# Optimization experiments

Measured on AMD Instinct MI355X. Metric: run time of the kernel, lower is better.

Reference implementation:

```python
import jax, jax.numpy as jnp
import numpy as np

K = 10

def _lrelu(v):
    return jax.nn.leaky_relu(v, negative_slope=0.2)

def _knn_idx(x, k):
    # x: [B, C, N]; returns indices of k nearest neighbors [B, N, k]
    xx = jnp.sum(x * x, axis=1, keepdims=True)          # [B,1,N]
    inner = -2.0 * jnp.einsum('bcn,bcm->bnm', x, x)     # [B,N,N]
    pd = -xx - inner - jnp.swapaxes(xx, 1, 2)           # -squared distance [B,N,N]
    _, idx = jax.lax.top_k(pd, k)
    return idx

def _graph_feature(x, k):
    # x: [B, C, N] -> edge features [B, 2C, N, k]
    idx = _knn_idx(x, k)                                # [B,N,k]
    xt = jnp.swapaxes(x, 1, 2)                          # [B,N,C]
    feat = jax.vmap(lambda xb, ib: xb[ib])(xt, idx)     # [B,N,k,C] gather
    center = xt[:, :, None, :]                          # [B,N,1,C]
    f = jnp.concatenate([feat - center,
                         jnp.broadcast_to(center, feat.shape)], axis=-1)  # [B,N,k,2C]
    return jnp.transpose(f, (0, 3, 1, 2))               # [B,2C,N,k]

def _edge_block(x, W, k):
    # conv2d 1x1 (no bias) + LeakyReLU + max over neighbors
    g = _graph_feature(x, k)                            # [B,2C,N,k]
    h = _lrelu(jnp.einsum('oc,bcnk->bonk', W, g))
    return jnp.max(h, axis=-1)                          # [B,O,N]

def setup_inputs() -> dict:
    key = jax.random.key(0)
    ks = jax.random.split(key, 9)
    def w(k_, *shape):
        fan_in = shape[-1]
        return jax.random.normal(k_, shape, dtype=jnp.float32) / np.sqrt(fan_in)
    return {
        'x':  jax.random.normal(ks[0], (8, 3, 2048), dtype=jnp.float32),
        'W1': w(ks[1], 64, 6),
        'W2': w(ks[2], 64, 128),
        'W3': w(ks[3], 128, 128),
        'W4': w(ks[4], 256, 256),
        'W5': w(ks[5], 512, 512),
        'L1': w(ks[6], 512, 1024),
        'L2': w(ks[7], 256, 512),
        'b2': jnp.zeros((256,), dtype=jnp.float32),
    }

def reference(x, W1, W2, W3, W4, W5, L1, L2, b2):
    x1 = _edge_block(x,  W1, K)   # [B,64,N]
    x2 = _edge_block(x1, W2, K)   # [B,64,N]
    x3 = _edge_block(x2, W3, K)   # [B,128,N]
    x4 = _edge_block(x3, W4, K)   # [B,256,N]
    h = jnp.concatenate([x1, x2, x3, x4], axis=1)        # [B,512,N]
    h = _lrelu(jnp.einsum('oc,bcn->bon', W5, h))         # [B,512,N]
    hmax = jnp.max(h, axis=-1)                           # [B,512]
    havg = jnp.mean(h, axis=-1)                          # [B,512]
    f = jnp.concatenate([hmax, havg], axis=1)            # [B,1024]
    f = _lrelu(f @ L1.T)                                 # [B,512]
    out = _lrelu(f @ L2.T + b2)                          # [B,256]
    return out
```

## Files before the change

kernel.cpp:

```cpp
#include <hip/hip_runtime.h>
#include <cstdint>
#include <cstddef>

constexpr int B_ = 8;
constexpr int N_ = 2048;
constexpr int K_ = 10;

typedef __attribute__((ext_vector_type(8))) short bf16x8;
typedef __attribute__((ext_vector_type(4))) float f32x4;

__device__ __forceinline__ float lrelu(float v) { return fmaxf(v, 0.2f * v); }

__device__ __forceinline__ short f2bf(float f) {
    uint32_t u = __builtin_bit_cast(uint32_t, f);
    u += 0x7fff + ((u >> 16) & 1);
    return (short)(u >> 16);
}
__device__ __forceinline__ float bf2f(short s) {
    uint32_t x = ((uint32_t)(unsigned short)s) << 16;
    return __builtin_bit_cast(float, x);
}

__global__ void k_transpose(const float* __restrict__ x, float* __restrict__ xt) {
    int i = blockIdx.x * 256 + threadIdx.x;
    if (i >= B_ * N_) return;
    int b = i / N_, n = i % N_;
#pragma unroll
    for (int c = 0; c < 3; ++c)
        xt[(size_t)i * 3 + c] = x[((size_t)b * 3 + c) * N_ + n];
}

__global__ void k_cvt(const float* __restrict__ W4, const float* __restrict__ W5,
                      short* __restrict__ Wb4, short* __restrict__ W5b) {
    int i = blockIdx.x * 256 + threadIdx.x;
    if (i < 256 * 128) {
        Wb4[i] = f2bf(W4[(size_t)(i >> 7) * 256 + (i & 127)]);
    } else {
        int k = i - 256 * 128;
        if (k < 512 * 512) W5b[k] = f2bf(W5[k]);
    }
}

__global__ void k_cvt2(const float* __restrict__ W2, const float* __restrict__ W3,
                       short* __restrict__ w2h, short* __restrict__ w2l,
                       short* __restrict__ w3h, short* __restrict__ w3l) {
    int i = blockIdx.x * 256 + threadIdx.x;
    if (i < 64 * 64) {
        float v = W2[(size_t)(i >> 6) * 128 + (i & 63)];
        short h = f2bf(v);
        w2h[i] = h; w2l[i] = f2bf(v - bf2f(h));
    } else if (i < 64 * 64 + 128 * 64) {
        int k = i - 64 * 64;
        float v = W3[(size_t)(k >> 6) * 128 + (k & 63)];
        short h = f2bf(v);
        w3h[k] = h; w3l[k] = f2bf(v - bf2f(h));
    }
}

__global__ void k_norms(const float* __restrict__ xt, int LD, int OFF, int C,
                        float* __restrict__ nrm) {
    int gid = blockIdx.x * 256 + threadIdx.x;
    int wid = gid >> 6;
    int lane = threadIdx.x & 63;
    if (wid >= B_ * N_) return;
    const float* row = xt + (size_t)wid * LD + OFF;
    float s = 0.f;
    for (int c = lane; c < C; c += 64) { float v = row[c]; s += v * v; }
#pragma unroll
    for (int off = 32; off; off >>= 1) s += __shfl_down(s, off);
    if (lane == 0) nrm[wid] = s;
}

__global__ __launch_bounds__(256) void k_knn3(const float* __restrict__ x,
                                              int* __restrict__ idxout) {
    __shared__ float xs[3][N_];
    __shared__ float ns[N_];
    const int b = blockIdx.x;
    const int w = threadIdx.x >> 6, lane = threadIdx.x & 63;
    const int n = blockIdx.y * 4 + w;
    for (int e = threadIdx.x; e < 3 * N_; e += 256)
        xs[e / N_][e % N_] = x[(size_t)b * 3 * N_ + e];
    __syncthreads();
    for (int m = threadIdx.x; m < N_; m += 256) {
        float a0 = xs[0][m], a1 = xs[1][m], a2 = xs[2][m];
        ns[m] = a0 * a0 + a1 * a1 + a2 * a2;
    }
    __syncthreads();
    const float q0 = xs[0][n], q1 = xs[1][n], q2 = xs[2][n];

    float sv[32];
#pragma unroll
    for (int g = 0; g < 32; ++g) {
        int m = g * 64 + lane;
        sv[g] = 2.f * (q0 * xs[0][m] + q1 * xs[1][m] + q2 * xs[2][m]) - ns[m];
    }
    float lm = sv[0];
#pragma unroll
    for (int g = 1; g < 32; ++g) lm = fmaxf(lm, sv[g]);
    float cur = lm, T = lm;
#pragma unroll
    for (int i = 0; i < K_; ++i) {
        float wm = cur;
#pragma unroll
        for (int off = 1; off < 64; off <<= 1) wm = fmaxf(wm, __shfl_xor(wm, off));
        T = wm;
        unsigned long long m = __ballot(cur == wm);
        int first = __ffsll(m) - 1;
        if (lane == first) cur = -INFINITY;
    }
    float kv[K_]; int ki[K_];
#pragma unroll
    for (int i = 0; i < K_; ++i) { kv[i] = -INFINITY; ki[i] = 0x7fffffff; }
#pragma unroll
    for (int g = 0; g < 32; ++g) {
        unsigned long long mk = __ballot(sv[g] >= T && sv[g] > kv[0]);
        while (mk) {
            int l = __ffsll(mk) - 1;
            mk &= mk - 1;
            float v = __shfl(sv[g], l);
            if (v > kv[0]) {
                kv[0] = v; ki[0] = g * 64 + l;
#pragma unroll
                for (int u = 0; u < K_ - 1; ++u)
                    if (kv[u] > kv[u + 1]) {
                        float tv = kv[u]; kv[u] = kv[u + 1]; kv[u + 1] = tv;
                        int tix = ki[u]; ki[u] = ki[u + 1]; ki[u + 1] = tix;
                    }
            }
        }
    }
    if (lane == 0) {
        int* op = idxout + ((size_t)b * N_ + n) * K_;
#pragma unroll
        for (int k = 0; k < K_; ++k) op[k] = ki[K_ - 1 - k];
    }
}

template <int C>
__global__ __launch_bounds__(256) void k_scores_mfma(const float* __restrict__ xt, int LD, int OFF,
                                                     const float* __restrict__ nrm,
                                                     float* __restrict__ S, int b0) {
    constexpr int RPC = C / 64;
    constexpr int NCH = 3 * RPC;
    constexpr int T = N_ / 64;
    __shared__ short AN[64 * 64];
    __shared__ short AM[64 * 64];
    const int bl = blockIdx.x;
    const int b = b0 + bl;
    int p = blockIdx.y;
    int r0 = 0, off = 0;
    while (off + (T - r0) <= p) { off += T - r0; ++r0; }
    const int ti = r0, tj = r0 + (p - off);
    const int n0 = ti * 64, m0 = tj * 64;
    const int t = threadIdx.x;
    const int lane = t & 63, w = t >> 6;
    const int colg = lane & 15, kg = lane >> 4;
    const float* xb = xt + ((size_t)b * N_) * LD + OFF;
    const float* nb = nrm + (size_t)b * N_;
    float* Sb = S + (size_t)bl * N_ * N_;

    f32x4 acc[4];
#pragma unroll
    for (int j = 0; j < 4; ++j) acc[j] = (f32x4){0.f, 0.f, 0.f, 0.f};

    for (int ch = 0; ch < NCH; ++ch) {
        const int region = ch / RPC;
        const int cc0 = (ch % RPC) * 64;
        __syncthreads();
#pragma unroll
        for (int e = 0; e < 4; ++e) {
            int idx = t + e * 256;
            int r = idx >> 4, q = idx & 15;
            float4 vn = *(const float4*)&xb[(size_t)(n0 + r) * LD + cc0 + q * 4];
            float4 vm = *(const float4*)&xb[(size_t)(m0 + r) * LD + cc0 + q * 4];
            float an4[4] = {vn.x, vn.y, vn.z, vn.w};
            float am4[4] = {vm.x, vm.y, vm.z, vm.w};
            short sa[4], sb[4];
#pragma unroll
            for (int c2 = 0; c2 < 4; ++c2) {
                short hn = f2bf(an4[c2]);
                short hm = f2bf(am4[c2]);
                sa[c2] = (region == 1) ? f2bf(an4[c2] - bf2f(hn)) : hn;
                sb[c2] = (region == 2) ? f2bf(am4[c2] - bf2f(hm)) : hm;
            }
            int base16 = r * 128 + (q >> 1) * 16;
            int byte = (base16 ^ ((r & 7) << 4)) + (q & 1) * 8;
            *(short4*)((char*)AN + byte) = make_short4(sa[0], sa[1], sa[2], sa[3]);
            *(short4*)((char*)AM + byte) = make_short4(sb[0], sb[1], sb[2], sb[3]);
        }
        __syncthreads();
        const int arow = w * 16 + colg;
#pragma unroll
        for (int s = 0; s < 2; ++s) {
            int abyte = (arow * 128 + s * 64 + kg * 16) ^ ((arow & 7) << 4);
            bf16x8 af = *(const bf16x8*)((const char*)AN + abyte);
#pragma unroll
            for (int j = 0; j < 4; ++j) {
                int brow = j * 16 + colg;
                int bbyte = (brow * 128 + s * 64 + kg * 16) ^ ((brow & 7) << 4);
                bf16x8 bfr = *(const bf16x8*)((const char*)AM + bbyte);
                acc[j] = __builtin_amdgcn_mfma_f32_16x16x32_bf16(af, bfr, acc[j], 0, 0, 0);
            }
        }
    }
#pragma unroll
    for (int j = 0; j < 4; ++j) {
        float nm = nb[m0 + j * 16 + colg];
#pragma unroll
        for (int r = 0; r < 4; ++r) {
            int row = n0 + w * 16 + kg * 4 + r;
            Sb[(size_t)row * N_ + m0 + j * 16 + colg] = 2.f * acc[j][r] - nm;
        }
    }
    if (ti != tj) {
#pragma unroll
        for (int r = 0; r < 4; ++r) {
            int nrow = n0 + w * 16 + kg * 4 + r;
            float nn = nb[nrow];
#pragma unroll
            for (int j = 0; j < 4; ++j)
                Sb[(size_t)(m0 + j * 16 + colg) * N_ + nrow] = 2.f * acc[j][r] - nn;
        }
    }
}

__global__ __launch_bounds__(256) void k_topk(const float* __restrict__ S,
                                              int* __restrict__ idxout, int b0) {
    const int bl = blockIdx.x, b = b0 + bl;
    const int wv = threadIdx.x >> 6, lane = threadIdx.x & 63;
    const int n = blockIdx.y * 4 + wv;
    const float* row = S + (size_t)bl * N_ * N_ + (size_t)n * N_;

    float sv[32];
#pragma unroll
    for (int g = 0; g < 32; ++g) sv[g] = __builtin_nontemporal_load(&row[g * 64 + lane]);

    float lm = sv[0];
#pragma unroll
    for (int g = 1; g < 32; ++g) lm = fmaxf(lm, sv[g]);

    float cur = lm, T = lm;
#pragma unroll
    for (int i = 0; i < K_; ++i) {
        float wm = cur;
#pragma unroll
        for (int off = 1; off < 64; off <<= 1) wm = fmaxf(wm, __shfl_xor(wm, off));
        T = wm;
        unsigned long long m = __ballot(cur == wm);
        int first = __ffsll(m) - 1;
        if (lane == first) cur = -INFINITY;
    }

    float kv[K_]; int ki[K_];
#pragma unroll
    for (int i = 0; i < K_; ++i) { kv[i] = -INFINITY; ki[i] = 0x7fffffff; }

#pragma unroll
    for (int g = 0; g < 32; ++g) {
        unsigned long long mk = __ballot(sv[g] >= T && sv[g] > kv[0]);
        while (mk) {
            int l = __ffsll(mk) - 1;
            mk &= mk - 1;
            float v = __shfl(sv[g], l);
            if (v > kv[0]) {
                kv[0] = v; ki[0] = g * 64 + l;
#pragma unroll
                for (int u = 0; u < K_ - 1; ++u)
                    if (kv[u] > kv[u + 1]) {
                        float tv = kv[u]; kv[u] = kv[u + 1]; kv[u + 1] = tv;
                        int tix = ki[u]; ki[u] = ki[u + 1]; ki[u + 1] = tix;
                    }
            }
        }
    }
    if (lane == 0) {
        int* op = idxout + ((size_t)b * N_ + n) * K_;
#pragma unroll
        for (int k = 0; k < K_; ++k) op[k] = ki[K_ - 1 - k];
    }
}

template <int C, int O>
__global__ __launch_bounds__(256) void k_center(const float* __restrict__ xt, int LD, int OFF,
                                                const float* __restrict__ W,
                                                float* __restrict__ tbuf) {
    constexpr int KC = (C == 3) ? 4 : 32;
    __shared__ __align__(16) float XT[64][36];
    __shared__ __align__(16) float WDT[KC][68];
    const int b = blockIdx.x;
    const int n0 = blockIdx.y * 64;
    const int ob = blockIdx.z * 64;
    const int t = threadIdx.x;
    const int tn = t & 15, to = t >> 4;
    const float* xb = xt + ((size_t)b * N_) * LD + OFF;
    float4 acc[4];
#pragma unroll
    for (int i = 0; i < 4; ++i) acc[i] = make_float4(0, 0, 0, 0);
    for (int c0 = 0; c0 < C; c0 += KC) {
        __syncthreads();
        for (int e = t; e < 64 * KC; e += 256) {
            int r = e / KC, cc = e % KC;
            XT[r][cc] = (C == 3) ? ((cc < 3) ? xb[(size_t)(n0 + r) * LD + cc] : 0.f)
                                 : xb[(size_t)(n0 + r) * LD + c0 + cc];
        }
        for (int e = t; e < 64 * KC; e += 256) {
            int oo = e / KC, cc = e % KC;
            float wd, wc;
            if (C == 3) {
                wd = (cc < 3) ? W[(ob + oo) * 6 + cc] : 0.f;
                wc = (cc < 3) ? W[(ob + oo) * 6 + 3 + cc] : 0.f;
            } else {
                wd = W[(size_t)(ob + oo) * (2 * C) + c0 + cc];
                wc = W[(size_t)(ob + oo) * (2 * C) + C + c0 + cc];
            }
            WDT[cc][oo] = wc - wd;
        }
        __syncthreads();
#pragma unroll 4
        for (int cc = 0; cc < KC; ++cc) {
            float4 w4 = *(const float4*)&WDT[cc][to * 4];
#pragma unroll
            for (int i = 0; i < 4; ++i) {
                float a = XT[tn * 4 + i][cc];
                acc[i].x += a * w4.x; acc[i].y += a * w4.y;
                acc[i].z += a * w4.z; acc[i].w += a * w4.w;
            }
        }
    }
#pragma unroll
    for (int i = 0; i < 4; ++i)
        *(float4*)&tbuf[((size_t)b * N_ + n0 + tn * 4 + i) * O + ob + to * 4] = acc[i];
}

template <int C, int O>
__global__ __launch_bounds__(256) void k_conv(const float* __restrict__ xt, int LDI, int OFFI,
                                              const int* __restrict__ idx,
                                              const float* __restrict__ W,
                                              const float* __restrict__ tbuf,
                                              float* __restrict__ hout, int OFFO) {
    constexpr int KC = (C == 3) ? 4 : 32;
    __shared__ __align__(16) float A[160][36];
    __shared__ __align__(16) float WT[KC][68];
    __shared__ int nb_s[160];
    const int b = blockIdx.x;
    const int n0 = blockIdx.y * 16;
    const int t = threadIdx.x;
    const int p = t >> 4, og = t & 15;
    if (t < 160) nb_s[t] = idx[((size_t)b * N_ + n0 + t / K_) * K_ + (t % K_)];
    const float* xb = xt + ((size_t)b * N_) * LDI + OFFI;

    for (int ob = 0; ob < O; ob += 64) {
        float4 acc[K_];
#pragma unroll
        for (int j = 0; j < K_; ++j) acc[j] = make_float4(0, 0, 0, 0);
        for (int c0 = 0; c0 < C; c0 += KC) {
            __syncthreads();
            if (C == 3) {
                for (int e = t; e < 160 * 4; e += 256) {
                    int r = e / 4, cc = e % 4;
                    A[r][cc] = (cc < 3) ? xb[(size_t)nb_s[r] * LDI + cc] : 0.f;
                }
            } else {
                for (int e = t; e < 160 * 8; e += 256) {
                    int r = e / 8, c4 = e % 8;
                    *(float4*)&A[r][c4 * 4] =
                        *(const float4*)&xb[(size_t)nb_s[r] * LDI + c0 + c4 * 4];
                }
            }
            for (int e = t; e < 64 * KC; e += 256) {
                int oo = e / KC, cc = e % KC;
                float w;
                if (C == 3) w = (cc < 3) ? W[(ob + oo) * 6 + cc] : 0.f;
                else        w = W[(size_t)(ob + oo) * (2 * C) + c0 + cc];
                WT[cc][oo] = w;
            }
            __syncthreads();
#pragma unroll 4
            for (int cc = 0; cc < KC; ++cc) {
                float4 w4 = *(const float4*)&WT[cc][og * 4];
#pragma unroll
                for (int j = 0; j < K_; ++j) {
                    float a = A[p * K_ + j][cc];
                    acc[j].x += a * w4.x; acc[j].y += a * w4.y;
                    acc[j].z += a * w4.z; acc[j].w += a * w4.w;
                }
            }
        }
        float4 tv = *(const float4*)&tbuf[((size_t)b * N_ + n0 + p) * O + ob + og * 4];
        float4 mx = acc[0];
#pragma unroll
        for (int j = 1; j < K_; ++j) {
            mx.x = fmaxf(mx.x, acc[j].x); mx.y = fmaxf(mx.y, acc[j].y);
            mx.z = fmaxf(mx.z, acc[j].z); mx.w = fmaxf(mx.w, acc[j].w);
        }
        float4 r;
        r.x = lrelu(mx.x + tv.x); r.y = lrelu(mx.y + tv.y);
        r.z = lrelu(mx.z + tv.z); r.w = lrelu(mx.w + tv.w);
        *(float4*)&hout[((size_t)b * N_ + n0 + p) * 512 + OFFO + ob + og * 4] = r;
    }
}

template <int O>
__global__ __launch_bounds__(256) void k_conv23_mfma(const float* __restrict__ hcat, int OFFI,
                                                     const int* __restrict__ idx,
                                                     const short* __restrict__ Wh,
                                                     const short* __restrict__ Wl,
                                                     const float* __restrict__ tbuf,
                                                     float* __restrict__ hout, int OFFO) {
    constexpr int CT = O / 64;
    __shared__ short Ah[160 * 64];
    __shared__ short Al[160 * 64];
    __shared__ int nb_s[160];
    const int b = blockIdx.x;
    const int n0 = blockIdx.y * 16;
    const int t = threadIdx.x;
    const int lane = t & 63, wv = t >> 6;
    const int colg = lane & 15, kg = lane >> 4;
    if (t < 160) nb_s[t] = idx[((size_t)b * N_ + n0 + t / K_) * K_ + (t % K_)];
    __syncthreads();
    for (int e = t; e < 160 * 16; e += 256) {
        int r = e >> 4, q = e & 15;
        const float4 v = *(const float4*)&hcat[((size_t)b * N_ + nb_s[r]) * 512 + OFFI + q * 4];
        float a4[4] = {v.x, v.y, v.z, v.w};
        short sh[4], sl[4];
#pragma unroll
        for (int c2 = 0; c2 < 4; ++c2) {
            sh[c2] = f2bf(a4[c2]);
            sl[c2] = f2bf(a4[c2] - bf2f(sh[c2]));
        }
        int byte = r * 128 + ((q * 8) ^ (((r / K_) & 7) << 4));
        *(short4*)((char*)Ah + byte) = make_short4(sh[0], sh[1], sh[2], sh[3]);
        *(short4*)((char*)Al + byte) = make_short4(sl[0], sl[1], sl[2], sl[3]);
    }
    bf16x8 bh[CT][2], blo[CT][2];
    const int obase = wv * (O / 4);
#pragma unroll
    for (int ct = 0; ct < CT; ++ct)
#pragma unroll
        for (int ks = 0; ks < 2; ++ks) {
            int o = obase + ct * 16 + colg;
            bh[ct][ks]  = *(const bf16x8*)&Wh[(size_t)o * 64 + ks * 32 + kg * 8];
            blo[ct][ks] = *(const bf16x8*)&Wl[(size_t)o * 64 + ks * 32 + kg * 8];
        }
    __syncthreads();

    f32x4 macc[CT];
#pragma unroll
    for (int ct = 0; ct < CT; ++ct)
        macc[ct] = (f32x4){-INFINITY, -INFINITY, -INFINITY, -INFINITY};

    const int aswz = (colg & 7) << 4;
#pragma unroll
    for (int j = 0; j < K_; ++j) {
        const int arow = colg * K_ + j;
        bf16x8 afh[2], afl[2];
#pragma unroll
        for (int ks = 0; ks < 2; ++ks) {
            int byte = arow * 128 + ((ks * 64 + kg * 16) ^ aswz);
            afh[ks] = *(const bf16x8*)((const char*)Ah + byte);
            afl[ks] = *(const bf16x8*)((const char*)Al + byte);
        }
        f32x4 acc[CT];
#pragma unroll
        for (int ct = 0; ct < CT; ++ct) acc[ct] = (f32x4){0.f, 0.f, 0.f, 0.f};
#pragma unroll
        for (int ks = 0; ks < 2; ++ks)
#pragma unroll
            for (int ct = 0; ct < CT; ++ct)
                acc[ct] = __builtin_amdgcn_mfma_f32_16x16x32_bf16(afh[ks], bh[ct][ks], acc[ct], 0, 0, 0);
#pragma unroll
        for (int ks = 0; ks < 2; ++ks)
#pragma unroll
            for (int ct = 0; ct < CT; ++ct)
                acc[ct] = __builtin_amdgcn_mfma_f32_16x16x32_bf16(afl[ks], bh[ct][ks], acc[ct], 0, 0, 0);
#pragma unroll
        for (int ks = 0; ks < 2; ++ks)
#pragma unroll
            for (int ct = 0; ct < CT; ++ct)
                acc[ct] = __builtin_amdgcn_mfma_f32_16x16x32_bf16(afh[ks], blo[ct][ks], acc[ct], 0, 0, 0);
#pragma unroll
        for (int ct = 0; ct < CT; ++ct) {
            macc[ct].x = fmaxf(macc[ct].x, acc[ct].x);
            macc[ct].y = fmaxf(macc[ct].y, acc[ct].y);
            macc[ct].z = fmaxf(macc[ct].z, acc[ct].z);
            macc[ct].w = fmaxf(macc[ct].w, acc[ct].w);
        }
    }
#pragma unroll
    for (int ct = 0; ct < CT; ++ct)
#pragma unroll
        for (int r = 0; r < 4; ++r) {
            int p = kg * 4 + r;
            int o = obase + ct * 16 + colg;
            float v = macc[ct][r] + tbuf[((size_t)b * N_ + n0 + p) * O + o];
            hout[((size_t)b * N_ + n0 + p) * 512 + OFFO + o] = lrelu(v);
        }
}

__global__ __launch_bounds__(256) void k_conv4_mfma(const float* __restrict__ hcat,
                                                    const int* __restrict__ idx,
                                                    const short* __restrict__ Wb,
                                                    const float* __restrict__ tbuf,
                                                    float* __restrict__ hout) {
    __shared__ short Ab[160 * 128];
    __shared__ int nb_s[160];
    const int b = blockIdx.x;
    const int n0 = blockIdx.y * 16;
    const int t = threadIdx.x;
    const int lane = t & 63, wv = t >> 6;
    const int colg = lane & 15, kg = lane >> 4;
    if (t < 160) nb_s[t] = idx[((size_t)b * N_ + n0 + t / K_) * K_ + (t % K_)];
    __syncthreads();
    for (int e = t; e < 160 * 32; e += 256) {
        int r = e >> 5, q = e & 31;
        const float4 v = *(const float4*)&hcat[((size_t)b * N_ + nb_s[r]) * 512 + 128 + q * 4];
        short4 s4 = { f2bf(v.x), f2bf(v.y), f2bf(v.z), f2bf(v.w) };
        int byte = r * 256 + ((q * 8) ^ (((r / K_) & 7) << 4));
        *(short4*)((char*)Ab + byte) = s4;
    }
    bf16x8 bf[4][4];
    const int ob = wv * 64;
#pragma unroll
    for (int nt = 0; nt < 4; ++nt)
#pragma unroll
        for (int ks = 0; ks < 4; ++ks)
            bf[nt][ks] = *(const bf16x8*)&Wb[(size_t)(ob + nt * 16 + colg) * 128 + ks * 32 + kg * 8];
    __syncthreads();

    f32x4 macc[4];
#pragma unroll
    for (int nt = 0; nt < 4; ++nt)
        macc[nt] = (f32x4){-INFINITY, -INFINITY, -INFINITY, -INFINITY};

    const int arow = colg * K_;
    const int aswz = (colg & 7) << 4;
#pragma unroll
    for (int j = 0; j < K_; ++j) {
        f32x4 acc[4];
#pragma unroll
        for (int nt = 0; nt < 4; ++nt) acc[nt] = (f32x4){0.f, 0.f, 0.f, 0.f};
#pragma unroll
        for (int ks = 0; ks < 4; ++ks) {
            int byte = (arow + j) * 256 + (((ks * 32 + kg * 8) * 2) ^ aswz);
            bf16x8 af = *(const bf16x8*)((const char*)Ab + byte);
#pragma unroll
            for (int nt = 0; nt < 4; ++nt)
                acc[nt] = __builtin_amdgcn_mfma_f32_16x16x32_bf16(af, bf[nt][ks], acc[nt], 0, 0, 0);
        }
#pragma unroll
        for (int nt = 0; nt < 4; ++nt) {
            macc[nt].x = fmaxf(macc[nt].x, acc[nt].x);
            macc[nt].y = fmaxf(macc[nt].y, acc[nt].y);
            macc[nt].z = fmaxf(macc[nt].z, acc[nt].z);
            macc[nt].w = fmaxf(macc[nt].w, acc[nt].w);
        }
    }
#pragma unroll
    for (int nt = 0; nt < 4; ++nt)
#pragma unroll
        for (int r = 0; r < 4; ++r) {
            int p = kg * 4 + r;
            int o = ob + nt * 16 + colg;
            float v = macc[nt][r] + tbuf[((size_t)b * N_ + n0 + p) * 256 + o];
            hout[((size_t)b * N_ + n0 + p) * 512 + 256 + o] = lrelu(v);
        }
}

__global__ __launch_bounds__(256) void k_final_mfma(const float* __restrict__ hcat,
                                                    const short* __restrict__ W5b,
                                                    float* __restrict__ pmax,
                                                    float* __restrict__ psum) {
    __shared__ short Ab[64 * 128];
    const int b = blockIdx.x, nc = blockIdx.y, obk = blockIdx.z;
    const int n0 = nc * 64, ob = obk * 64;
    const int t = threadIdx.x, lane = t & 63, wv = t >> 6;
    const int colg = lane & 15, kg = lane >> 4;
    const int o = ob + wv * 16 + colg;

    f32x4 acc[4];
#pragma unroll
    for (int mt = 0; mt < 4; ++mt) acc[mt] = (f32x4){0.f, 0.f, 0.f, 0.f};

    for (int kc = 0; kc < 4; ++kc) {
        __syncthreads();
        for (int e = t; e < 64 * 32; e += 256) {
            int r = e >> 5, q = e & 31;
            const float4 v = *(const float4*)&hcat[((size_t)b * N_ + n0 + r) * 512 + kc * 128 + q * 4];
            short4 s4 = { f2bf(v.x), f2bf(v.y), f2bf(v.z), f2bf(v.w) };
            int byte = r * 256 + ((q * 8) ^ ((r & 7) << 4));
            *(short4*)((char*)Ab + byte) = s4;
        }
        __syncthreads();
#pragma unroll
        for (int ks = 0; ks < 4; ++ks) {
            bf16x8 bfrag = *(const bf16x8*)&W5b[(size_t)o * 512 + kc * 128 + ks * 32 + kg * 8];
#pragma unroll
            for (int mt = 0; mt < 4; ++mt) {
                int row = mt * 16 + colg;
                int byte = row * 256 + (((ks * 32 + kg * 8) * 2) ^ ((row & 7) << 4));
                bf16x8 af = *(const bf16x8*)((const char*)Ab + byte);
                acc[mt] = __builtin_amdgcn_mfma_f32_16x16x32_bf16(af, bfrag, acc[mt], 0, 0, 0);
            }
        }
    }
    float mx = -INFINITY, sm = 0.f;
#pragma unroll
    for (int mt = 0; mt < 4; ++mt)
#pragma unroll
        for (int r = 0; r < 4; ++r) {
            float v = lrelu(acc[mt][r]);
            mx = fmaxf(mx, v); sm += v;
        }
    mx = fmaxf(mx, __shfl_xor(mx, 16)); sm += __shfl_xor(sm, 16);
    mx = fmaxf(mx, __shfl_xor(mx, 32)); sm += __shfl_xor(sm, 32);
    if (lane < 16) {
        pmax[((size_t)b * 512 + ob + wv * 16 + lane) * 32 + nc] = mx;
        psum[((size_t)b * 512 + ob + wv * 16 + lane) * 32 + nc] = sm;
    }
}

__global__ __launch_bounds__(256) void k_pool(const float* __restrict__ pmax,
                                              const float* __restrict__ psum,
                                              float* __restrict__ f) {
    int i = blockIdx.x * 256 + threadIdx.x;
    if (i >= B_ * 512) return;
    int b = i >> 9, o = i & 511;
    const float* pm = pmax + (size_t)i * 32;
    const float* ps = psum + (size_t)i * 32;
    float mm = -INFINITY, ss = 0.f;
#pragma unroll
    for (int q = 0; q < 32; ++q) { mm = fmaxf(mm, pm[q]); ss += ps[q]; }
    f[(size_t)b * 1024 + o] = mm;
    f[(size_t)b * 1024 + 512 + o] = ss * (1.0f / 2048.0f);
}

__global__ __launch_bounds__(256) void k_fc1(const float* __restrict__ f,
                                             const float* __restrict__ L1,
                                             float* __restrict__ f1) {
    __shared__ float fs[8][1024];
    const int t = threadIdx.x, lane = t & 63, w = t >> 6;
    for (int e = t; e < 2048; e += 256)
        *(float4*)&fs[0][e * 4] = *(const float4*)&f[e * 4];
    __syncthreads();
    const int o = blockIdx.x * 4 + w;
    float acc[8];
#pragma unroll
    for (int b = 0; b < 8; ++b) acc[b] = 0.f;
    const float* Lrow = L1 + (size_t)o * 1024;
#pragma unroll
    for (int e = 0; e < 16; ++e) {
        float wv = Lrow[e * 64 + lane];
#pragma unroll
        for (int b = 0; b < 8; ++b) acc[b] += wv * fs[b][e * 64 + lane];
    }
#pragma unroll
    for (int off = 32; off; off >>= 1)
#pragma unroll
        for (int b = 0; b < 8; ++b) acc[b] += __shfl_xor(acc[b], off);
#pragma unroll
    for (int b = 0; b < 8; ++b)
        if (lane == b) f1[(size_t)b * 512 + o] = lrelu(acc[b]);
}

__global__ __launch_bounds__(256) void k_fc2(const float* __restrict__ f1,
                                             const float* __restrict__ L2,
                                             const float* __restrict__ b2,
                                             float* __restrict__ out) {
    __shared__ float fs[8][512];
    const int t = threadIdx.x, lane = t & 63, w = t >> 6;
    for (int e = t; e < 1024; e += 256)
        *(float4*)&fs[0][e * 4] = *(const float4*)&f1[e * 4];
    __syncthreads();
    const int o = blockIdx.x * 4 + w;
    float acc[8];
#pragma unroll
    for (int b = 0; b < 8; ++b) acc[b] = 0.f;
    const float* Lrow = L2 + (size_t)o * 512;
#pragma unroll
    for (int e = 0; e < 8; ++e) {
        float wv = Lrow[e * 64 + lane];
#pragma unroll
        for (int b = 0; b < 8; ++b) acc[b] += wv * fs[b][e * 64 + lane];
    }
#pragma unroll
    for (int off = 32; off; off >>= 1)
#pragma unroll
        for (int b = 0; b < 8; ++b) acc[b] += __shfl_xor(acc[b], off);
    float bb = b2[o];
#pragma unroll
    for (int b = 0; b < 8; ++b)
        if (lane == b) out[(size_t)b * 256 + o] = lrelu(acc[b] + bb);
}

extern "C" void kernel_launch(void* const* d_in, const int* in_sizes, int n_in,
                              void* d_out, int out_size, void* d_ws, size_t ws_size,
                              hipStream_t stream) {
    (void)in_sizes; (void)n_in; (void)out_size;
    const float* x  = (const float*)d_in[0];
    const float* W1 = (const float*)d_in[1];
    const float* W2 = (const float*)d_in[2];
    const float* W3 = (const float*)d_in[3];
    const float* W4 = (const float*)d_in[4];
    const float* W5 = (const float*)d_in[5];
    const float* L1 = (const float*)d_in[6];
    const float* L2 = (const float*)d_in[7];
    const float* b2 = (const float*)d_in[8];
    float* out = (float*)d_out;

    float* ws   = (float*)d_ws;
    float* xt   = ws;
    float* nrm  = xt + (size_t)B_ * N_ * 3;
    int*   idxb = (int*)(nrm + (size_t)B_ * N_);
    float* tb   = (float*)(idxb + (size_t)B_ * N_ * K_);
    float* hcat = tb + (size_t)B_ * N_ * 256;
    float* pmax = hcat + (size_t)B_ * N_ * 512;
    float* psum = pmax + (size_t)B_ * 512 * 32;
    short* wb4  = (short*)(psum + (size_t)B_ * 512 * 32);
    short* w5b  = wb4 + 256 * 128;
    short* w2h  = w5b + 512 * 512;
    short* w2l  = w2h + 64 * 64;
    short* w3h  = w2l + 64 * 64;
    short* w3l  = w3h + 128 * 64;
    float* fbuf = (float*)(w3l + 128 * 64);
    float* f1b  = fbuf + 8192;
    float* scor = f1b + 4096;

    const size_t base_f = 49152 + 16384 + 163840 + 4194304 + 8388608 +
                          131072 + 131072 + 16384 + 131072 + 12288 + 8192 + 4096;
    const size_t nsq = (size_t)N_ * N_;
    size_t avail = (ws_size / 4 > base_f) ? (ws_size / 4 - base_f) : 0;
    int CH = 1;
    if (avail >= 8 * nsq) CH = 8;
    else if (avail >= 4 * nsq) CH = 4;
    else if (avail >= 2 * nsq) CH = 2;

    constexpr int TP = (N_ / 64) * (N_ / 64 + 1) / 2;

    dim3 blk(256);
    k_transpose<<<dim3((B_ * N_ + 255) / 256), blk, 0, stream>>>(x, xt);
    k_cvt<<<dim3((256 * 128 + 512 * 512 + 255) / 256), blk, 0, stream>>>(W4, W5, wb4, w5b);
    k_cvt2<<<dim3((64 * 64 + 128 * 64 + 255) / 256), blk, 0, stream>>>(W2, W3, w2h, w2l, w3h, w3l);

    k_knn3<<<dim3(B_, N_ / 4), blk, 0, stream>>>(x, idxb);
    k_center<3, 64><<<dim3(B_, N_ / 64, 1), blk, 0, stream>>>(xt, 3, 0, W1, tb);
    k_conv<3, 64><<<dim3(B_, N_ / 16), blk, 0, stream>>>(xt, 3, 0, idxb, W1, tb, hcat, 0);

    k_norms<<<dim3(B_ * N_ / 4), blk, 0, stream>>>(hcat, 512, 0, 64, nrm);
    for (int b0 = 0; b0 < B_; b0 += CH) {
        k_scores_mfma<64><<<dim3(CH, TP), blk, 0, stream>>>(hcat, 512, 0, nrm, scor, b0);
        k_topk<<<dim3(CH, N_ / 4), blk, 0, stream>>>(scor, idxb, b0);
    }
    k_center<64, 64><<<dim3(B_, N_ / 64, 1), blk, 0, stream>>>(hcat, 512, 0, W2, tb);
    k_conv23_mfma<64><<<dim3(B_, N_ / 16), blk, 0, stream>>>(hcat, 0, idxb, w2h, w2l, tb, hcat, 64);

    k_norms<<<dim3(B_ * N_ / 4), blk, 0, stream>>>(hcat, 512, 64, 64, nrm);
    for (int b0 = 0; b0 < B_; b0 += CH) {
        k_scores_mfma<64><<<dim3(CH, TP), blk, 0, stream>>>(hcat, 512, 64, nrm, scor, b0);
        k_topk<<<dim3(CH, N_ / 4), blk, 0, stream>>>(scor, idxb, b0);
    }
    k_center<64, 128><<<dim3(B_, N_ / 64, 2), blk, 0, stream>>>(hcat, 512, 64, W3, tb);
    k_conv23_mfma<128><<<dim3(B_, N_ / 16), blk, 0, stream>>>(hcat, 64, idxb, w3h, w3l, tb, hcat, 128);

    k_norms<<<dim3(B_ * N_ / 4), blk, 0, stream>>>(hcat, 512, 128, 128, nrm);
    for (int b0 = 0; b0 < B_; b0 += CH) {
        k_scores_mfma<128><<<dim3(CH, TP), blk, 0, stream>>>(hcat, 512, 128, nrm, scor, b0);
        k_topk<<<dim3(CH, N_ / 4), blk, 0, stream>>>(scor, idxb, b0);
    }
    k_center<128, 256><<<dim3(B_, N_ / 64, 4), blk, 0, stream>>>(hcat, 512, 128, W4, tb);
    k_conv4_mfma<<<dim3(B_, N_ / 16), blk, 0, stream>>>(hcat, idxb, wb4, tb, hcat);

    k_final_mfma<<<dim3(B_, 32, 8), blk, 0, stream>>>(hcat, w5b, pmax, psum);
    k_pool<<<dim3(B_ * 512 / 256), blk, 0, stream>>>(pmax, psum, fbuf);
    k_fc1<<<dim3(128), blk, 0, stream>>>(fbuf, L1, f1b);
    k_fc2<<<dim3(64), blk, 0, stream>>>(f1b, L2, b2, out);
}
```

Before: 524.0 us.

## Store kNN score matrix in bf16 and rerank candidates with exact fp32 distances

The pairwise score matrix written by the MFMA score kernel is now stored as bf16 instead of fp32, halving the N×N write and read traffic. The top-k kernel finds the 10th-largest bf16 score as a threshold. It then recomputes exact fp32 dot products against hcat for every candidate at or above that threshold, and selects the final neighbours from those exact values. The halved buffer also lets more batches fit per chunk. The risk is extra gather and shuffle-reduce work when many candidates tie near the threshold, plus possible misses if bf16 rounding pushes a true neighbour below the threshold.

```diff
diff --git a/kernel.cpp b/kernel.cpp
--- a/kernel.cpp
+++ b/kernel.cpp
@@ -18,6 +18,10 @@
 }
 __device__ __forceinline__ float bf2f(short s) {
     uint32_t x = ((uint32_t)(unsigned short)s) << 16;
+    return __builtin_bit_cast(float, x);
+}
+__device__ __forceinline__ float bf2fu(unsigned short u) {
+    uint32_t x = ((uint32_t)u) << 16;
     return __builtin_bit_cast(float, x);
 }
 
@@ -139,7 +143,7 @@
 template <int C>
 __global__ __launch_bounds__(256) void k_scores_mfma(const float* __restrict__ xt, int LD, int OFF,
                                                      const float* __restrict__ nrm,
-                                                     float* __restrict__ S, int b0) {
+                                                     unsigned short* __restrict__ S, int b0) {
     constexpr int RPC = C / 64;
     constexpr int NCH = 3 * RPC;
     constexpr int T = N_ / 64;
@@ -157,7 +161,7 @@
     const int colg = lane & 15, kg = lane >> 4;
     const float* xb = xt + ((size_t)b * N_) * LD + OFF;
     const float* nb = nrm + (size_t)b * N_;
-    float* Sb = S + (size_t)bl * N_ * N_;
+    unsigned short* Sb = S + (size_t)bl * N_ * N_;
 
     f32x4 acc[4];
 #pragma unroll
@@ -209,7 +213,7 @@
 #pragma unroll
         for (int r = 0; r < 4; ++r) {
             int row = n0 + w * 16 + kg * 4 + r;
-            Sb[(size_t)row * N_ + m0 + j * 16 + colg] = 2.f * acc[j][r] - nm;
+            Sb[(size_t)row * N_ + m0 + j * 16 + colg] = (unsigned short)f2bf(2.f * acc[j][r] - nm);
         }
     }
     if (ti != tj) {
@@ -219,26 +223,35 @@
             float nn = nb[nrow];
 #pragma unroll
             for (int j = 0; j < 4; ++j)
-                Sb[(size_t)(m0 + j * 16 + colg) * N_ + nrow] = 2.f * acc[j][r] - nn;
-        }
-    }
-}
-
-__global__ __launch_bounds__(256) void k_topk(const float* __restrict__ S,
+                Sb[(size_t)(m0 + j * 16 + colg) * N_ + nrow] = (unsigned short)f2bf(2.f * acc[j][r] - nn);
+        }
+    }
+}
+
+template <int C>
+__global__ __launch_bounds__(256) void k_topk(const unsigned short* __restrict__ S,
+                                              const float* __restrict__ hcat, int LD, int OFF,
+                                              const float* __restrict__ nrm,
                                               int* __restrict__ idxout, int b0) {
     const int bl = blockIdx.x, b = b0 + bl;
     const int wv = threadIdx.x >> 6, lane = threadIdx.x & 63;
     const int n = blockIdx.y * 4 + wv;
-    const float* row = S + (size_t)bl * N_ * N_ + (size_t)n * N_;
-
-    float sv[32];
-#pragma unroll
-    for (int g = 0; g < 32; ++g) sv[g] = __builtin_nontemporal_load(&row[g * 64 + lane]);
-
-    float lm = sv[0];
-#pragma unroll
-    for (int g = 1; g < 32; ++g) lm = fmaxf(lm, sv[g]);
-
+    const unsigned short* row = S + (size_t)bl * N_ * N_ + (size_t)n * N_;
+
+    float sv[8][4];
+#pragma unroll
+    for (int g = 0; g < 8; ++g) {
+        uint2 u = *(const uint2*)&row[g * 256 + lane * 4];
+        sv[g][0] = bf2fu((unsigned short)(u.x & 0xffffu));
+        sv[g][1] = bf2fu((unsigned short)(u.x >> 16));
+        sv[g][2] = bf2fu((unsigned short)(u.y & 0xffffu));
+        sv[g][3] = bf2fu((unsigned short)(u.y >> 16));
+    }
+    float lm = sv[0][0];
+#pragma unroll
+    for (int g = 0; g < 8; ++g)
+#pragma unroll
+        for (int e = 0; e < 4; ++e) lm = fmaxf(lm, sv[g][e]);
     float cur = lm, T = lm;
 #pragma unroll
     for (int i = 0; i < K_; ++i) {
@@ -250,33 +263,77 @@
         int first = __ffsll(m) - 1;
         if (lane == first) cur = -INFINITY;
     }
-
-    float kv[K_]; int ki[K_];
-#pragma unroll
-    for (int i = 0; i < K_; ++i) { kv[i] = -INFINITY; ki[i] = 0x7fffffff; }
-
-#pragma unroll
-    for (int g = 0; g < 32; ++g) {
-        unsigned long long mk = __ballot(sv[g] >= T && sv[g] > kv[0]);
+    float kv[K_];
+#pragma unroll
+    for (int i = 0; i < K_; ++i) kv[i] = -INFINITY;
+#pragma unroll
+    for (int g = 0; g < 8; ++g) {
+        float m4 = fmaxf(fmaxf(sv[g][0], sv[g][1]), fmaxf(sv[g][2], sv[g][3]));
+        unsigned long long mk = __ballot(m4 >= T && m4 > kv[0]);
         while (mk) {
             int l = __ffsll(mk) - 1;
             mk &= mk - 1;
-            float v = __shfl(sv[g], l);
-            if (v > kv[0]) {
-                kv[0] = v; ki[0] = g * 64 + l;
-#pragma unroll
-                for (int u = 0; u < K_ - 1; ++u)
-                    if (kv[u] > kv[u + 1]) {
-                        float tv = kv[u]; kv[u] = kv[u + 1]; kv[u + 1] = tv;
-                        int tix = ki[u]; ki[u] = ki[u + 1]; ki[u + 1] = tix;
+            float v0 = __shfl(sv[g][0], l), v1 = __shfl(sv[g][1], l);
+            float v2 = __shfl(sv[g][2], l), v3 = __shfl(sv[g][3], l);
+            float vb[4] = {v0, v1, v2, v3};
+#pragma unroll
+            for (int e = 0; e < 4; ++e) {
+                float v = vb[e];
+                if (v >= T && v > kv[0]) {
+                    kv[0] = v;
+#pragma unroll
+                    for (int u = 0; u < K_ - 1; ++u)
+                        if (kv[u] > kv[u + 1]) { float tv = kv[u]; kv[u] = kv[u + 1]; kv[u + 1] = tv; }
+                }
+            }
+        }
+    }
+    const float Tb10 = kv[0];
+    const float* hq = hcat + ((size_t)b * N_ + n) * LD + OFF;
+    float xq0 = hq[lane];
+    float xq1 = (C == 128) ? hq[64 + lane] : 0.f;
+    const float* nb = nrm + (size_t)b * N_;
+    float kv2[K_]; int ki2[K_];
+#pragma unroll
+    for (int i = 0; i < K_; ++i) { kv2[i] = -INFINITY; ki2[i] = 0x7fffffff; }
+#pragma unroll
+    for (int g = 0; g < 8; ++g) {
+        float m4 = fmaxf(fmaxf(sv[g][0], sv[g][1]), fmaxf(sv[g][2], sv[g][3]));
+        unsigned long long mk = __ballot(m4 >= Tb10);
+        while (mk) {
+            int l = __ffsll(mk) - 1;
+            mk &= mk - 1;
+            float v0 = __shfl(sv[g][0], l), v1 = __shfl(sv[g][1], l);
+            float v2 = __shfl(sv[g][2], l), v3 = __shfl(sv[g][3], l);
+            float vb[4] = {v0, v1, v2, v3};
+            const int base = g * 256 + l * 4;
+#pragma unroll
+            for (int e = 0; e < 4; ++e) {
+                if (vb[e] >= Tb10) {
+                    int m = base + e;
+                    const float* hm = hcat + ((size_t)b * N_ + m) * LD + OFF;
+                    float pr = xq0 * hm[lane];
+                    if (C == 128) pr += xq1 * hm[64 + lane];
+#pragma unroll
+                    for (int off = 1; off < 64; off <<= 1) pr += __shfl_xor(pr, off);
+                    float s = 2.f * pr - nb[m];
+                    if (s > kv2[0]) {
+                        kv2[0] = s; ki2[0] = m;
+#pragma unroll
+                        for (int u = 0; u < K_ - 1; ++u)
+                            if (kv2[u] > kv2[u + 1]) {
+                                float tv = kv2[u]; kv2[u] = kv2[u + 1]; kv2[u + 1] = tv;
+                                int ti2 = ki2[u]; ki2[u] = ki2[u + 1]; ki2[u + 1] = ti2;
+                            }
                     }
+                }
             }
         }
     }
     if (lane == 0) {
         int* op = idxout + ((size_t)b * N_ + n) * K_;
 #pragma unroll
-        for (int k = 0; k < K_; ++k) op[k] = ki[K_ - 1 - k];
+        for (int k = 0; k < K_; ++k) op[k] = ki2[K_ - 1 - k];
     }
 }
 
@@ -723,16 +780,16 @@
     short* w3l  = w3h + 128 * 64;
     float* fbuf = (float*)(w3l + 128 * 64);
     float* f1b  = fbuf + 8192;
-    float* scor = f1b + 4096;
+    unsigned short* scor = (unsigned short*)(f1b + 4096);
 
     const size_t base_f = 49152 + 16384 + 163840 + 4194304 + 8388608 +
                           131072 + 131072 + 16384 + 131072 + 12288 + 8192 + 4096;
     const size_t nsq = (size_t)N_ * N_;
     size_t avail = (ws_size / 4 > base_f) ? (ws_size / 4 - base_f) : 0;
     int CH = 1;
-    if (avail >= 8 * nsq) CH = 8;
-    else if (avail >= 4 * nsq) CH = 4;
-    else if (avail >= 2 * nsq) CH = 2;
+    if (avail >= 8 * nsq / 2) CH = 8;
+    else if (avail >= 4 * nsq / 2) CH = 4;
+    else if (avail >= 2 * nsq / 2) CH = 2;
 
     constexpr int TP = (N_ / 64) * (N_ / 64 + 1) / 2;
 
@@ -748,7 +805,7 @@
     k_norms<<<dim3(B_ * N_ / 4), blk, 0, stream>>>(hcat, 512, 0, 64, nrm);
     for (int b0 = 0; b0 < B_; b0 += CH) {
         k_scores_mfma<64><<<dim3(CH, TP), blk, 0, stream>>>(hcat, 512, 0, nrm, scor, b0);
-        k_topk<<<dim3(CH, N_ / 4), blk, 0, stream>>>(scor, idxb, b0);
+        k_topk<64><<<dim3(CH, N_ / 4), blk, 0, stream>>>(scor, hcat, 512, 0, nrm, idxb, b0);
     }
     k_center<64, 64><<<dim3(B_, N_ / 64, 1), blk, 0, stream>>>(hcat, 512, 0, W2, tb);
     k_conv23_mfma<64><<<dim3(B_, N_ / 16), blk, 0, stream>>>(hcat, 0, idxb, w2h, w2l, tb, hcat, 64);
@@ -756,7 +813,7 @@
     k_norms<<<dim3(B_ * N_ / 4), blk, 0, stream>>>(hcat, 512, 64, 64, nrm);
     for (int b0 = 0; b0 < B_; b0 += CH) {
         k_scores_mfma<64><<<dim3(CH, TP), blk, 0, stream>>>(hcat, 512, 64, nrm, scor, b0);
-        k_topk<<<dim3(CH, N_ / 4), blk, 0, stream>>>(scor, idxb, b0);
+        k_topk<64><<<dim3(CH, N_ / 4), blk, 0, stream>>>(scor, hcat, 512, 64, nrm, idxb, b0);
     }
     k_center<64, 128><<<dim3(B_, N_ / 64, 2), blk, 0, stream>>>(hcat, 512, 64, W3, tb);
     k_conv23_mfma<128><<<dim3(B_, N_ / 16), blk, 0, stream>>>(hcat, 64, idxb, w3h, w3l, tb, hcat, 128);
@@ -764,7 +821,7 @@
     k_norms<<<dim3(B_ * N_ / 4), blk, 0, stream>>>(hcat, 512, 128, 128, nrm);
     for (int b0 = 0; b0 < B_; b0 += CH) {
         k_scores_mfma<128><<<dim3(CH, TP), blk, 0, stream>>>(hcat, 512, 128, nrm, scor, b0);
-        k_topk<<<dim3(CH, N_ / 4), blk, 0, stream>>>(scor, idxb, b0);
+        k_topk<128><<<dim3(CH, N_ / 4), blk, 0, stream>>>(scor, hcat, 512, 128, nrm, idxb, b0);
     }
     k_center<128, 256><<<dim3(B_, N_ / 64, 4), blk, 0, stream>>>(hcat, 512, 128, W4, tb);
     k_conv4_mfma<<<dim3(B_, N_ / 16), blk, 0, stream>>>(hcat, idxb, wb4, tb, hcat);
```

New measurement: 609.2 us. +16.3%, slower.
